# Kernel optimization log

Measured on AMD Instinct MI355X. Metric: run time of the kernel, lower is better.

Reference implementation:

```python
import jax, jax.numpy as jnp
import numpy as np

B, N, M = 8192, 4096, 4096  # batch tokens, input_size, output_size


def setup_inputs() -> dict:
    key = jax.random.key(0)
    k1, k2, k3, k4, k5 = jax.random.split(key, 5)
    x = jax.random.normal(k1, (B, N), dtype=jnp.float32)
    W_m = jax.random.normal(k2, (N, M), dtype=jnp.float32) * 0.001
    W_u = jnp.full((N,), np.log(0.01), dtype=jnp.float32) + 0.01 * jax.random.normal(k3, (N,), dtype=jnp.float32)
    W_v = jnp.full((M,), np.log(0.01), dtype=jnp.float32) + 0.01 * jax.random.normal(k4, (M,), dtype=jnp.float32)
    eps = jax.random.normal(k5, (N, M), dtype=jnp.float32)
    return {"x": x, "W_m": W_m, "W_u": W_u, "W_v": W_v, "eps": eps}


def reference(x, W_m, W_u, W_v, eps):
    # diag(exp(0.5*u)) @ eps @ diag(exp(0.5*v)) == row/col elementwise scaling
    W = W_m + jnp.exp(0.5 * W_u)[:, None] * eps * jnp.exp(0.5 * W_v)[None, :]
    return x @ W  # [B, M]; original forward never adds bias
```

## Files before the change

kernel.cpp:

```cpp
#include <hip/hip_runtime.h>
#include <hip/hip_bf16.h>

typedef short bf16x8 __attribute__((ext_vector_type(8)));
typedef short short8 __attribute__((ext_vector_type(8)));
typedef float f32x4  __attribute__((ext_vector_type(4)));

__device__ __forceinline__ short f2bf(float f) {
    union { float f; unsigned u; } a; a.f = f;
    unsigned r = a.u + 0x7fffu + ((a.u >> 16) & 1u);
    return (short)(r >> 16);
}

__device__ __forceinline__ void gload16(const void* g, void* l) {
    __builtin_amdgcn_global_load_lds(
        (const __attribute__((address_space(1))) unsigned int*)g,
        (__attribute__((address_space(3))) unsigned int*)l,
        16, 0, 0);
}

__global__ __launch_bounds__(256) void cvt_x(const float* __restrict__ x,
                                             short* __restrict__ xb, long n) {
    const long t = (long)blockIdx.x * blockDim.x + threadIdx.x;
    const long stride = (long)gridDim.x * blockDim.x;
    for (long i = t * 8; i < n; i += stride * 8) {
        float4 v0 = *(const float4*)&x[i];
        float4 v1 = *(const float4*)&x[i + 4];
        short8 o;
        o[0] = f2bf(v0.x); o[1] = f2bf(v0.y); o[2] = f2bf(v0.z); o[3] = f2bf(v0.w);
        o[4] = f2bf(v1.x); o[5] = f2bf(v1.y); o[6] = f2bf(v1.z); o[7] = f2bf(v1.w);
        *(short8*)&xb[i] = o;
    }
}

__global__ __launch_bounds__(256) void build_wt(const float* __restrict__ Wm,
                                                const float* __restrict__ eps,
                                                const float* __restrict__ Wu,
                                                const float* __restrict__ Wv,
                                                short* __restrict__ Wt,
                                                int N, int M) {
    __shared__ __align__(16) short tile[64][68];
    __shared__ float su[64], sv[64];
    const int n0 = blockIdx.y * 64, m0 = blockIdx.x * 64;
    const int t = threadIdx.x;
    if (t < 64)        su[t]      = __expf(0.5f * Wu[n0 + t]);
    else if (t < 128)  sv[t - 64] = __expf(0.5f * Wv[m0 + t - 64]);
    __syncthreads();
    for (int c = t; c < 1024; c += 256) {
        const int row = c >> 4, c4 = c & 15;
        const long g = (long)(n0 + row) * M + m0 + c4 * 4;
        float4 wm = *(const float4*)&Wm[g];
        float4 ep = *(const float4*)&eps[g];
        const float s = su[row];
        short4 o;
        o.x = f2bf(wm.x + s * ep.x * sv[c4 * 4 + 0]);
        o.y = f2bf(wm.y + s * ep.y * sv[c4 * 4 + 1]);
        o.z = f2bf(wm.z + s * ep.z * sv[c4 * 4 + 2]);
        o.w = f2bf(wm.w + s * ep.w * sv[c4 * 4 + 3]);
        *(short4*)&tile[row][c4 * 4] = o;
    }
    __syncthreads();
    for (int c = t; c < 512; c += 256) {
        const int mm = c >> 3, nn8 = (c & 7) * 8;
        bf16x8 o;
        #pragma unroll
        for (int j = 0; j < 8; ++j) o[j] = tile[nn8 + j][mm];
        *(bf16x8*)&Wt[(long)(m0 + mm) * N + n0 + nn8] = o;
    }
}

#define KDIM 4096

template<int BUF, int MH, int NH>
__device__ __forceinline__ void phase_loads(const char* sm, int aoff, int boff,
                                            int c0, int c1,
                                            bf16x8 (&a)[4][2], bf16x8 (&b)[2][2]) {
    const char* pa = sm + BUF * 32768 + MH * 16384 + aoff;
    const char* pb = sm + 65536 + BUF * 32768 + NH * 16384 + boff;
    #pragma unroll
    for (int mf = 0; mf < 4; ++mf) {
        a[mf][0] = *(const bf16x8*)(pa + mf * 2048 + c0);
        a[mf][1] = *(const bf16x8*)(pa + mf * 2048 + c1);
    }
    #pragma unroll
    for (int nf = 0; nf < 2; ++nf) {
        b[nf][0] = *(const bf16x8*)(pb + nf * 2048 + c0);
        b[nf][1] = *(const bf16x8*)(pb + nf * 2048 + c1);
    }
}

template<int MH, int NH>
__device__ __forceinline__ void phase_mfma(const bf16x8 (&a)[4][2], const bf16x8 (&b)[2][2],
                                           f32x4 (&acc)[8][4]) {
    #pragma unroll
    for (int mf = 0; mf < 4; ++mf)
        #pragma unroll
        for (int nf = 0; nf < 2; ++nf)
            #pragma unroll
            for (int ks = 0; ks < 2; ++ks)
                acc[MH * 4 + mf][NH * 2 + nf] = __builtin_amdgcn_mfma_f32_16x16x32_bf16(
                    a[mf][ks], b[nf][ks], acc[MH * 4 + mf][NH * 2 + nf], 0, 0, 0);
}

__device__ __forceinline__ void stage2(const short* g, char* l) {
    gload16(g, l);
    gload16(g + 8 * KDIM, l + 1024);
}

__global__ __launch_bounds__(512, 2) void gemm256(const short* __restrict__ A,
                                                  const short* __restrict__ Bt,
                                                  float* __restrict__ C) {
    __shared__ __align__(16) char smem[131072];
    const char* smc = smem;

    const int tid = threadIdx.x;
    const int wid = tid >> 6, lane = tid & 63;
    const int wm = wid >> 2, wn = wid & 3;
    const int l15 = lane & 15, l4 = lane >> 4;

    const int bsw = (blockIdx.x & 7) * 64 + (blockIdx.x >> 3);
    const int bx = bsw & 15, by = bsw >> 4;
    const int brow = by * 256, bcol = bx * 256;

    const int s7 = l15 & 7;
    const int c0 = ((l4) ^ s7) * 16;
    const int c1 = ((l4 + 4) ^ s7) * 16;
    const int aoff = (wm * 64 + l15) * 128;
    const int boff = (wn * 32 + l15) * 128;

    const int p0 = wid * 128 + lane;
    const int srow = p0 >> 3;
    const int sk = (p0 & 7) ^ (srow & 7);
    const short* gA = A  + (long)(brow + srow) * KDIM + sk * 8;
    const short* gB = Bt + (long)(bcol + srow) * KDIM + sk * 8;
    char* smw = smem + wid * 2048;

#define STAGE_A(BUF, H, T) stage2(gA + (H) * (128 * KDIM) + (T) * 64, smw + (BUF) * 32768 + (H) * 16384)
#define STAGE_B(BUF, H, T) stage2(gB + (H) * (128 * KDIM) + (T) * 64, smw + 65536 + (BUF) * 32768 + (H) * 16384)

    f32x4 acc[8][4];
    #pragma unroll
    for (int i = 0; i < 8; ++i)
        #pragma unroll
        for (int j = 0; j < 4; ++j) acc[i][j] = {0.f, 0.f, 0.f, 0.f};

    STAGE_A(0, 0, 0);
    STAGE_B(0, 0, 0);
    STAGE_B(0, 1, 0);
    STAGE_A(0, 1, 0);
    STAGE_A(1, 0, 1);
    STAGE_B(1, 0, 1);
    asm volatile("s_waitcnt vmcnt(4)" ::: "memory");
    __builtin_amdgcn_s_barrier();

#define PHASE(BUF, MH, NH, STAGE_STMT, VM_STMT) {                          \
        bf16x8 afr[4][2], bfr[2][2];                                       \
        phase_loads<BUF, MH, NH>(smc, aoff, boff, c0, c1, afr, bfr);       \
        STAGE_STMT;                                                        \
        VM_STMT;                                                           \
        __builtin_amdgcn_s_barrier();                                      \
        asm volatile("s_waitcnt lgkmcnt(0)");                              \
        __builtin_amdgcn_s_setprio(1);                                     \
        phase_mfma<MH, NH>(afr, bfr, acc);                                 \
        __builtin_amdgcn_s_setprio(0);                                     \
        __builtin_amdgcn_s_barrier();                                      \
    }
#define VM4 asm volatile("s_waitcnt vmcnt(4)" ::: "memory")

    for (int it = 0; it < 32; ++it) {
        const int T = 2 * it;
        const int t1 = T + 1;
        const int t2 = (T + 2) & 63;
        const int t3 = (T + 3) & 63;
        PHASE(0, 0, 0, STAGE_B(1, 1, t1), );
        PHASE(0, 0, 1, STAGE_A(1, 1, t1), );
        PHASE(0, 1, 0, STAGE_A(0, 0, t2), );
        PHASE(0, 1, 1, STAGE_B(0, 0, t2), VM4);
        PHASE(1, 0, 0, STAGE_B(0, 1, t2), );
        PHASE(1, 0, 1, STAGE_A(0, 1, t2), );
        PHASE(1, 1, 0, STAGE_A(1, 0, t3), );
        PHASE(1, 1, 1, STAGE_B(1, 0, t3), VM4);
    }

    const int cr = l4 * 4;
    #pragma unroll
    for (int mh = 0; mh < 2; ++mh)
        #pragma unroll
        for (int mf = 0; mf < 4; ++mf) {
            const long row = brow + mh * 128 + wm * 64 + mf * 16 + cr;
            #pragma unroll
            for (int nh = 0; nh < 2; ++nh)
                #pragma unroll
                for (int nf = 0; nf < 2; ++nf) {
                    const long col = bcol + nh * 128 + wn * 32 + nf * 16 + l15;
                    const f32x4 v = acc[mh * 4 + mf][nh * 2 + nf];
                    float* p = C + row * 4096 + col;
                    p[0]        = v[0];
                    p[4096]     = v[1];
                    p[2 * 4096] = v[2];
                    p[3 * 4096] = v[3];
                }
        }
#undef PHASE
#undef VM4
#undef STAGE_A
#undef STAGE_B
}

extern "C" void kernel_launch(void* const* d_in, const int* in_sizes, int n_in,
                              void* d_out, int out_size, void* d_ws, size_t ws_size,
                              hipStream_t stream) {
    const float* x   = (const float*)d_in[0];
    const float* Wm  = (const float*)d_in[1];
    const float* Wu  = (const float*)d_in[2];
    const float* Wv  = (const float*)d_in[3];
    const float* eps = (const float*)d_in[4];
    float* out = (float*)d_out;

    const int N = in_sizes[2];
    const int M = in_sizes[3];
    const int B = in_sizes[0] / N;

    short* xb = (short*)d_ws;
    short* wt = (short*)((char*)d_ws + (size_t)B * N * 2);

    cvt_x<<<2048, 256, 0, stream>>>(x, xb, (long)B * N);
    build_wt<<<dim3(M / 64, N / 64), 256, 0, stream>>>(Wm, eps, Wu, Wv, wt, N, M);
    gemm256<<<dim3((B / 256) * (M / 256)), 512, 0, stream>>>(xb, wt, out);
}
```

Baseline: 558.0 us.

## Reuse A/B fragments across phases in serpentine order to cut LDS reads

Rewrites the 8-phase main loop so register fragments are reused between adjacent phases. Phases now visit quadrants in the order (0,0),(0,1),(1,1),(1,0), so only one of A or B is reloaded from LDS per phase after the first. This cuts ds_read traffic per K-tile roughly in half. The cost is more live registers for an extra B fragment set and a changed waitcnt and barrier schedule, which could pressure occupancy at 2 waves per SIMD.

```diff
diff --git a/kernel.cpp b/kernel.cpp
--- a/kernel.cpp
+++ b/kernel.cpp
@@ -70,17 +70,21 @@
 
 #define KDIM 4096
 
-template<int BUF, int MH, int NH>
-__device__ __forceinline__ void phase_loads(const char* sm, int aoff, int boff,
-                                            int c0, int c1,
-                                            bf16x8 (&a)[4][2], bf16x8 (&b)[2][2]) {
+template<int BUF, int MH>
+__device__ __forceinline__ void load_a(const char* sm, int aoff, int c0, int c1,
+                                       bf16x8 (&a)[4][2]) {
     const char* pa = sm + BUF * 32768 + MH * 16384 + aoff;
-    const char* pb = sm + 65536 + BUF * 32768 + NH * 16384 + boff;
     #pragma unroll
     for (int mf = 0; mf < 4; ++mf) {
         a[mf][0] = *(const bf16x8*)(pa + mf * 2048 + c0);
         a[mf][1] = *(const bf16x8*)(pa + mf * 2048 + c1);
     }
+}
+
+template<int BUF, int NH>
+__device__ __forceinline__ void load_b(const char* sm, int boff, int c0, int c1,
+                                       bf16x8 (&b)[2][2]) {
+    const char* pb = sm + 65536 + BUF * 32768 + NH * 16384 + boff;
     #pragma unroll
     for (int nf = 0; nf < 2; ++nf) {
         b[nf][0] = *(const bf16x8*)(pb + nf * 2048 + c0);
@@ -89,8 +93,8 @@
 }
 
 template<int MH, int NH>
-__device__ __forceinline__ void phase_mfma(const bf16x8 (&a)[4][2], const bf16x8 (&b)[2][2],
-                                           f32x4 (&acc)[8][4]) {
+__device__ __forceinline__ void do_mfma(const bf16x8 (&a)[4][2], const bf16x8 (&b)[2][2],
+                                        f32x4 (&acc)[8][4]) {
     #pragma unroll
     for (int mf = 0; mf < 4; ++mf)
         #pragma unroll
@@ -136,6 +140,12 @@
 
 #define STAGE_A(BUF, H, T) stage2(gA + (H) * (128 * KDIM) + (T) * 64, smw + (BUF) * 32768 + (H) * 16384)
 #define STAGE_B(BUF, H, T) stage2(gB + (H) * (128 * KDIM) + (T) * 64, smw + 65536 + (BUF) * 32768 + (H) * 16384)
+#define BAR   __builtin_amdgcn_s_barrier()
+#define LGKM0 asm volatile("s_waitcnt lgkmcnt(0)")
+#define LGKM8 asm volatile("s_waitcnt lgkmcnt(8)")
+#define VM4   asm volatile("s_waitcnt vmcnt(4)" ::: "memory")
+#define PRIO1 __builtin_amdgcn_s_setprio(1)
+#define PRIO0 __builtin_amdgcn_s_setprio(0)
 
     f32x4 acc[8][4];
     #pragma unroll
@@ -150,35 +160,57 @@
     STAGE_A(1, 0, 1);
     STAGE_B(1, 0, 1);
     asm volatile("s_waitcnt vmcnt(4)" ::: "memory");
-    __builtin_amdgcn_s_barrier();
-
-#define PHASE(BUF, MH, NH, STAGE_STMT, VM_STMT) {                          \
-        bf16x8 afr[4][2], bfr[2][2];                                       \
-        phase_loads<BUF, MH, NH>(smc, aoff, boff, c0, c1, afr, bfr);       \
-        STAGE_STMT;                                                        \
-        VM_STMT;                                                           \
-        __builtin_amdgcn_s_barrier();                                      \
-        asm volatile("s_waitcnt lgkmcnt(0)");                              \
-        __builtin_amdgcn_s_setprio(1);                                     \
-        phase_mfma<MH, NH>(afr, bfr, acc);                                 \
-        __builtin_amdgcn_s_setprio(0);                                     \
-        __builtin_amdgcn_s_barrier();                                      \
-    }
-#define VM4 asm volatile("s_waitcnt vmcnt(4)" ::: "memory")
+    BAR;
+
+    bf16x8 Afr[4][2], B0fr[2][2], B1fr[2][2];
 
     for (int it = 0; it < 32; ++it) {
         const int T = 2 * it;
         const int t1 = T + 1;
         const int t2 = (T + 2) & 63;
         const int t3 = (T + 3) & 63;
-        PHASE(0, 0, 0, STAGE_B(1, 1, t1), );
-        PHASE(0, 0, 1, STAGE_A(1, 1, t1), );
-        PHASE(0, 1, 0, STAGE_A(0, 0, t2), );
-        PHASE(0, 1, 1, STAGE_B(0, 0, t2), VM4);
-        PHASE(1, 0, 0, STAGE_B(0, 1, t2), );
-        PHASE(1, 0, 1, STAGE_A(0, 1, t2), );
-        PHASE(1, 1, 0, STAGE_A(1, 0, t3), );
-        PHASE(1, 1, 1, STAGE_B(1, 0, t3), VM4);
+
+        load_a<0, 0>(smc, aoff, c0, c1, Afr);
+        load_b<0, 0>(smc, boff, c0, c1, B0fr);
+        STAGE_B(1, 1, t1);
+        LGKM8; BAR; LGKM0;
+        PRIO1; do_mfma<0, 0>(Afr, B0fr, acc); PRIO0;
+        BAR;
+        load_b<0, 1>(smc, boff, c0, c1, B1fr);
+        STAGE_A(1, 1, t1);
+        BAR; LGKM0;
+        PRIO1; do_mfma<0, 1>(Afr, B1fr, acc); PRIO0;
+        BAR;
+        load_a<0, 1>(smc, aoff, c0, c1, Afr);
+        STAGE_A(0, 0, t2);
+        BAR; LGKM0;
+        PRIO1; do_mfma<1, 1>(Afr, B1fr, acc); PRIO0;
+        BAR;
+        STAGE_B(0, 0, t2);
+        VM4; BAR;
+        PRIO1; do_mfma<1, 0>(Afr, B0fr, acc); PRIO0;
+        BAR;
+
+        load_a<1, 0>(smc, aoff, c0, c1, Afr);
+        load_b<1, 0>(smc, boff, c0, c1, B0fr);
+        STAGE_B(0, 1, t2);
+        LGKM8; BAR; LGKM0;
+        PRIO1; do_mfma<0, 0>(Afr, B0fr, acc); PRIO0;
+        BAR;
+        load_b<1, 1>(smc, boff, c0, c1, B1fr);
+        STAGE_A(0, 1, t2);
+        BAR; LGKM0;
+        PRIO1; do_mfma<0, 1>(Afr, B1fr, acc); PRIO0;
+        BAR;
+        load_a<1, 1>(smc, aoff, c0, c1, Afr);
+        STAGE_A(1, 0, t3);
+        BAR; LGKM0;
+        PRIO1; do_mfma<1, 1>(Afr, B1fr, acc); PRIO0;
+        BAR;
+        STAGE_B(1, 0, t3);
+        VM4; BAR;
+        PRIO1; do_mfma<1, 0>(Afr, B0fr, acc); PRIO0;
+        BAR;
     }
 
     const int cr = l4 * 4;
@@ -200,10 +232,14 @@
                     p[3 * 4096] = v[3];
                 }
         }
-#undef PHASE
-#undef VM4
 #undef STAGE_A
 #undef STAGE_B
+#undef BAR
+#undef LGKM0
+#undef LGKM8
+#undef VM4
+#undef PRIO1
+#undef PRIO0
 }
 
 extern "C" void kernel_launch(void* const* d_in, const int* in_sizes, int n_in,
```

Result: faster. 537.3 us (-3.7%).
